# Kernel optimization log

Hardware: AMD Instinct MI355X
Metric: run time of the kernel (lower is better)

The kernel has to match this reference:

```python
import jax, jax.numpy as jnp
import numpy as np

B, S, D, H, OUT = 64, 2048, 1024, 300, 2
DROPOUT = 0.2


def setup_inputs() -> dict:
    key = jax.random.key(0)
    k_in, k_ids, k_pos, k_mask, k_w1, k_w2 = jax.random.split(key, 6)
    inputs = jax.random.normal(k_in, (B, S, D), dtype=jnp.float32)
    # token ids in [2, 32000); then plant a single '1' (EOS/pad marker) per row
    input_ids = jax.random.randint(k_ids, (B, S), 2, 32000, dtype=jnp.int64)
    eos_pos = jax.random.randint(k_pos, (B,), S // 2, S)
    input_ids = input_ids.at[jnp.arange(B), eos_pos].set(1)
    # realized Bernoulli(1 - dropout) token-keep mask, [B, S, 1]
    drop_mask = (jax.random.uniform(k_mask, (B, S, 1)) < (1.0 - DROPOUT)).astype(jnp.float32)
    W1 = jax.random.normal(k_w1, (H, D), dtype=jnp.float32) * 0.02
    b1 = jnp.zeros((H,), dtype=jnp.float32)
    W2 = jax.random.normal(k_w2, (OUT, H), dtype=jnp.float32) * 0.02
    b2 = jnp.zeros((OUT,), dtype=jnp.float32)
    return {"inputs": inputs, "input_ids": input_ids, "drop_mask": drop_mask,
            "W1": W1, "b1": b1, "W2": W2, "b2": b2}


def reference(inputs, input_ids, drop_mask, W1, b1, W2, b2):
    # end_ind[i] = first position where input_ids[i] == 1; fallback matches
    # the original's `except: end_ind = input_ids.shape[0]` (== batch size)
    is_end = input_ids == 1                              # [B, S]
    has_end = jnp.any(is_end, axis=1)                    # [B]
    first_end = jnp.argmax(is_end, axis=1)               # [B]
    end_ind = jnp.where(has_end, first_end, input_ids.shape[0])

    # masked, dropped segment-average over the first end_ind tokens
    valid = (jnp.arange(inputs.shape[1])[None, :] < end_ind[:, None])  # [B, S]
    weighted = inputs * drop_mask * valid[:, :, None].astype(inputs.dtype)
    euph = weighted.sum(axis=1) / end_ind[:, None].astype(inputs.dtype)  # [B, D]

    # 2-layer MLP with tanh
    hidden = jnp.tanh(euph @ W1.T + b1)
    out = hidden @ W2.T + b2                             # [B, 2]
    return out
```

## Files before the change

kernel.cpp:

```cpp
#include <hip/hip_runtime.h>
#include <math.h>

#define B 64
#define S 2048
#define D 1024
#define H 300
#define NOUT 2
#define NCHUNK 32
#define CHUNK_S (S / NCHUNK)

typedef float fx4 __attribute__((ext_vector_type(4)));

static __device__ __forceinline__ int imin(int a, int b) { return a < b ? a : b; }

__global__ __launch_bounds__(256) void end_kernel(const int* __restrict__ ids,
                                                  int* __restrict__ end_ind) {
    int b = blockIdx.x;
    int t = threadIdx.x;
    const int* row = ids + (size_t)b * S;
    int m = S;
    for (int s = t; s < S; s += 256) {
        if (row[s] == 1 && s < m) m = s;
    }
    __shared__ int red[256];
    red[t] = m;
    __syncthreads();
    for (int st = 128; st > 0; st >>= 1) {
        if (t < st) red[t] = imin(red[t], red[t + st]);
        __syncthreads();
    }
    if (t == 0) end_ind[b] = (red[0] < S) ? red[0] : B;
}

__global__ __launch_bounds__(256) void sum_partial_kernel(
        const float* __restrict__ inputs,
        const float* __restrict__ drop,
        const int* __restrict__ end_ind,
        float* __restrict__ partial ) {
    int chunk = blockIdx.x;
    int b = blockIdx.y;
    int t = threadIdx.x;

    __shared__ int   rows_l[CHUNK_S];
    __shared__ float w_l[CHUNK_S];
    __shared__ int   cnt_l;

    int e = end_ind[b];
    int s0 = chunk * CHUNK_S;
    int n = imin(s0 + CHUNK_S, e) - s0;

    if (t < 64) {
        float w = 0.f;
        if (t < n) w = drop[(size_t)b * S + s0 + t];
        unsigned long long mask = __ballot(w != 0.f);
        int pos = __popcll(mask & ((1ull << t) - 1ull));
        if (w != 0.f) { rows_l[pos] = t; w_l[pos] = w; }
        if (t == 0) cnt_l = __popcll(mask);
    }
    __syncthreads();

    int m = cnt_l;
    fx4 a0 = (fx4)(0.f);
    fx4 a1 = a0, a2 = a0, a3 = a0, a4 = a0, a5 = a0, a6 = a0, a7 = a0;

    const char* base = (const char*)inputs + (((size_t)b * S + s0) * D + 4 * (size_t)t) * sizeof(float);

    int i = 0;
    for (; i + 8 <= m; i += 8) {
        fx4 v0 = *(const fx4*)(base + ((size_t)rows_l[i + 0] << 12));
        fx4 v1 = *(const fx4*)(base + ((size_t)rows_l[i + 1] << 12));
        fx4 v2 = *(const fx4*)(base + ((size_t)rows_l[i + 2] << 12));
        fx4 v3 = *(const fx4*)(base + ((size_t)rows_l[i + 3] << 12));
        fx4 v4 = *(const fx4*)(base + ((size_t)rows_l[i + 4] << 12));
        fx4 v5 = *(const fx4*)(base + ((size_t)rows_l[i + 5] << 12));
        fx4 v6 = *(const fx4*)(base + ((size_t)rows_l[i + 6] << 12));
        fx4 v7 = *(const fx4*)(base + ((size_t)rows_l[i + 7] << 12));
        a0 += v0 * w_l[i + 0];
        a1 += v1 * w_l[i + 1];
        a2 += v2 * w_l[i + 2];
        a3 += v3 * w_l[i + 3];
        a4 += v4 * w_l[i + 4];
        a5 += v5 * w_l[i + 5];
        a6 += v6 * w_l[i + 6];
        a7 += v7 * w_l[i + 7];
    }
    for (; i < m; ++i) {
        fx4 v = *(const fx4*)(base + ((size_t)rows_l[i] << 12));
        a0 += v * w_l[i];
    }
    a0 = ((a0 + a1) + (a2 + a3)) + ((a4 + a5) + (a6 + a7));

    fx4* op = (fx4*)(partial + ((size_t)b * NCHUNK + chunk) * D) + t;
    *op = a0;
}

__global__ __launch_bounds__(256) void mlp_kernel(
        const float* __restrict__ partial,
        const int* __restrict__ end_ind,
        const float* __restrict__ W1, const float* __restrict__ b1,
        const float* __restrict__ W2, const float* __restrict__ b2,
        float* __restrict__ out) {
    int b = blockIdx.x;
    int t = threadIdx.x;
    int wave = t >> 6;
    int lane = t & 63;

    __shared__ fx4 x4[D / 4];
    __shared__ float hidden[H];
    __shared__ float red[256];

    float inv_e = 1.0f / (float)end_ind[b];
    {
        fx4 a = (fx4)(0.f);
        const fx4* p = (const fx4*)(partial + (size_t)b * NCHUNK * D) + t;
        for (int c = 0; c < NCHUNK; ++c, p += D / 4) {
            a += p[0];
        }
        x4[t] = a * inv_e;
    }
    __syncthreads();

    fx4 xr0 = x4[lane];
    fx4 xr1 = x4[lane + 64];
    fx4 xr2 = x4[lane + 128];
    fx4 xr3 = x4[lane + 192];

    for (int h = wave; h < H; h += 4) {
        const fx4* w = (const fx4*)(W1 + (size_t)h * D);
        fx4 acc = xr0 * w[lane]
                + xr1 * w[lane + 64]
                + xr2 * w[lane + 128]
                + xr3 * w[lane + 192];
        float d = acc.x + acc.y + acc.z + acc.w;
        #pragma unroll
        for (int mm = 32; mm > 0; mm >>= 1) d += __shfl_xor(d, mm, 64);
        if (lane == 0) hidden[h] = tanhf(d + b1[h]);
    }
    __syncthreads();

    for (int o = 0; o < NOUT; ++o) {
        float p = 0.f;
        for (int h = t; h < H; h += 256) p += hidden[h] * W2[(size_t)o * H + h];
        red[t] = p;
        __syncthreads();
        for (int st = 128; st > 0; st >>= 1) {
            if (t < st) red[t] += red[t + st];
            __syncthreads();
        }
        if (t == 0) out[b * NOUT + o] = red[0] + b2[o];
        __syncthreads();
    }
}

extern "C" void kernel_launch(void* const* d_in, const int* in_sizes, int n_in,
                              void* d_out, int out_size, void* d_ws, size_t ws_size,
                              hipStream_t stream) {
    const float* inputs = (const float*)d_in[0];
    const int*   ids    = (const int*)d_in[1];
    const float* drop   = (const float*)d_in[2];
    const float* W1     = (const float*)d_in[3];
    const float* b1v    = (const float*)d_in[4];
    const float* W2     = (const float*)d_in[5];
    const float* b2v    = (const float*)d_in[6];
    float* out = (float*)d_out;

    int*   end_ind = (int*)d_ws;
    float* partial = (float*)((char*)d_ws + 256);

    end_kernel<<<B, 256, 0, stream>>>(ids, end_ind);
    sum_partial_kernel<<<dim3(NCHUNK, B), 256, 0, stream>>>(inputs, drop, end_ind, partial);
    mlp_kernel<<<B, 256, 0, stream>>>(partial, end_ind, W1, b1v, W2, b2v, out);
}
```

Baseline: 733.2 us.

## Fuse end-index search into the sum kernel, halve chunk count, use nontemporal loads

Drops the separate end_kernel launch: every sum_partial block now scans the ids row itself, reduces the minimum with wave shuffles, and chunk 0 writes end_ind for the MLP kernel. Chunks grow from 64 to 128 rows, so row compaction is now built across two waves with a prefix offset. Input loads become nontemporal, and the MLP kernel runs with 512 threads so more W1 rows are handled in parallel. The cost is redundant id scans in every block and fewer, longer blocks, which may lower parallelism in the bandwidth-bound sum.

```diff
diff --git a/kernel.cpp b/kernel.cpp
--- a/kernel.cpp
+++ b/kernel.cpp
@@ -6,75 +6,79 @@
 #define D 1024
 #define H 300
 #define NOUT 2
-#define NCHUNK 32
+#define NCHUNK 16
 #define CHUNK_S (S / NCHUNK)
 
 typedef float fx4 __attribute__((ext_vector_type(4)));
 
 static __device__ __forceinline__ int imin(int a, int b) { return a < b ? a : b; }
 
-__global__ __launch_bounds__(256) void end_kernel(const int* __restrict__ ids,
-                                                  int* __restrict__ end_ind) {
-    int b = blockIdx.x;
-    int t = threadIdx.x;
-    const int* row = ids + (size_t)b * S;
-    int m = S;
-    for (int s = t; s < S; s += 256) {
-        if (row[s] == 1 && s < m) m = s;
-    }
-    __shared__ int red[256];
-    red[t] = m;
-    __syncthreads();
-    for (int st = 128; st > 0; st >>= 1) {
-        if (t < st) red[t] = imin(red[t], red[t + st]);
-        __syncthreads();
-    }
-    if (t == 0) end_ind[b] = (red[0] < S) ? red[0] : B;
-}
-
 __global__ __launch_bounds__(256) void sum_partial_kernel(
         const float* __restrict__ inputs,
+        const int* __restrict__ ids,
         const float* __restrict__ drop,
-        const int* __restrict__ end_ind,
+        int* __restrict__ end_ind,
         float* __restrict__ partial ) {
     int chunk = blockIdx.x;
     int b = blockIdx.y;
     int t = threadIdx.x;
+    int lane = t & 63;
+    int widx = t >> 6;
+
+    const int* idrow = ids + (size_t)b * S;
+    int m = S;
+    for (int s = t; s < S; s += 256) {
+        if (idrow[s] == 1 && s < m) m = s;
+    }
+    #pragma unroll
+    for (int off = 32; off > 0; off >>= 1) m = imin(m, __shfl_xor(m, off, 64));
+    __shared__ int wmin[4];
+    if (lane == 0) wmin[widx] = m;
+    __syncthreads();
+    int e_full = imin(imin(wmin[0], wmin[1]), imin(wmin[2], wmin[3]));
+    int e = (e_full < S) ? e_full : B;
+    if (t == 0 && chunk == 0) end_ind[b] = e;
+
+    int s0 = chunk * CHUNK_S;
+    int n = imin(s0 + CHUNK_S, e) - s0;
 
     __shared__ int   rows_l[CHUNK_S];
     __shared__ float w_l[CHUNK_S];
-    __shared__ int   cnt_l;
+    __shared__ int   wcnt[2];
 
-    int e = end_ind[b];
-    int s0 = chunk * CHUNK_S;
-    int n = imin(s0 + CHUNK_S, e) - s0;
-
-    if (t < 64) {
-        float w = 0.f;
-        if (t < n) w = drop[(size_t)b * S + s0 + t];
+    float w = 0.f;
+    int pos = 0;
+    if (t < CHUNK_S) {
+        w = (t < n) ? drop[(size_t)b * S + s0 + t] : 0.f;
         unsigned long long mask = __ballot(w != 0.f);
-        int pos = __popcll(mask & ((1ull << t) - 1ull));
-        if (w != 0.f) { rows_l[pos] = t; w_l[pos] = w; }
-        if (t == 0) cnt_l = __popcll(mask);
+        pos = __popcll(mask & ((1ull << lane) - 1ull));
+        if (lane == 0) wcnt[widx] = __popcll(mask);
     }
     __syncthreads();
+    int base0 = (widx == 1) ? wcnt[0] : 0;
+    if (t < CHUNK_S && w != 0.f) {
+        rows_l[base0 + pos] = t;
+        w_l[base0 + pos] = w;
+    }
+    int mtot = wcnt[0] + wcnt[1];
+    __syncthreads();
 
-    int m = cnt_l;
     fx4 a0 = (fx4)(0.f);
     fx4 a1 = a0, a2 = a0, a3 = a0, a4 = a0, a5 = a0, a6 = a0, a7 = a0;
 
-    const char* base = (const char*)inputs + (((size_t)b * S + s0) * D + 4 * (size_t)t) * sizeof(float);
+    const char* base = (const char*)inputs
+                     + (((size_t)b * S + s0) * D + 4 * (size_t)t) * sizeof(float);
 
     int i = 0;
-    for (; i + 8 <= m; i += 8) {
-        fx4 v0 = *(const fx4*)(base + ((size_t)rows_l[i + 0] << 12));
-        fx4 v1 = *(const fx4*)(base + ((size_t)rows_l[i + 1] << 12));
-        fx4 v2 = *(const fx4*)(base + ((size_t)rows_l[i + 2] << 12));
-        fx4 v3 = *(const fx4*)(base + ((size_t)rows_l[i + 3] << 12));
-        fx4 v4 = *(const fx4*)(base + ((size_t)rows_l[i + 4] << 12));
-        fx4 v5 = *(const fx4*)(base + ((size_t)rows_l[i + 5] << 12));
-        fx4 v6 = *(const fx4*)(base + ((size_t)rows_l[i + 6] << 12));
-        fx4 v7 = *(const fx4*)(base + ((size_t)rows_l[i + 7] << 12));
+    for (; i + 8 <= mtot; i += 8) {
+        fx4 v0 = __builtin_nontemporal_load((const fx4*)(base + ((size_t)rows_l[i + 0] << 12)));
+        fx4 v1 = __builtin_nontemporal_load((const fx4*)(base + ((size_t)rows_l[i + 1] << 12)));
+        fx4 v2 = __builtin_nontemporal_load((const fx4*)(base + ((size_t)rows_l[i + 2] << 12)));
+        fx4 v3 = __builtin_nontemporal_load((const fx4*)(base + ((size_t)rows_l[i + 3] << 12)));
+        fx4 v4 = __builtin_nontemporal_load((const fx4*)(base + ((size_t)rows_l[i + 4] << 12)));
+        fx4 v5 = __builtin_nontemporal_load((const fx4*)(base + ((size_t)rows_l[i + 5] << 12)));
+        fx4 v6 = __builtin_nontemporal_load((const fx4*)(base + ((size_t)rows_l[i + 6] << 12)));
+        fx4 v7 = __builtin_nontemporal_load((const fx4*)(base + ((size_t)rows_l[i + 7] << 12)));
         a0 += v0 * w_l[i + 0];
         a1 += v1 * w_l[i + 1];
         a2 += v2 * w_l[i + 2];
@@ -84,8 +88,8 @@
         a6 += v6 * w_l[i + 6];
         a7 += v7 * w_l[i + 7];
     }
-    for (; i < m; ++i) {
-        fx4 v = *(const fx4*)(base + ((size_t)rows_l[i] << 12));
+    for (; i < mtot; ++i) {
+        fx4 v = __builtin_nontemporal_load((const fx4*)(base + ((size_t)rows_l[i] << 12)));
         a0 += v * w_l[i];
     }
     a0 = ((a0 + a1) + (a2 + a3)) + ((a4 + a5) + (a6 + a7));
@@ -94,7 +98,7 @@
     *op = a0;
 }
 
-__global__ __launch_bounds__(256) void mlp_kernel(
+__global__ __launch_bounds__(512) void mlp_kernel(
         const float* __restrict__ partial,
         const int* __restrict__ end_ind,
         const float* __restrict__ W1, const float* __restrict__ b1,
@@ -107,10 +111,10 @@
 
     __shared__ fx4 x4[D / 4];
     __shared__ float hidden[H];
-    __shared__ float red[256];
+    __shared__ float red[512];
 
     float inv_e = 1.0f / (float)end_ind[b];
-    {
+    if (t < D / 4) {
         fx4 a = (fx4)(0.f);
         const fx4* p = (const fx4*)(partial + (size_t)b * NCHUNK * D) + t;
         for (int c = 0; c < NCHUNK; ++c, p += D / 4) {
@@ -125,7 +129,7 @@
     fx4 xr2 = x4[lane + 128];
     fx4 xr3 = x4[lane + 192];
 
-    for (int h = wave; h < H; h += 4) {
+    for (int h = wave; h < H; h += 8) {
         const fx4* w = (const fx4*)(W1 + (size_t)h * D);
         fx4 acc = xr0 * w[lane]
                 + xr1 * w[lane + 64]
@@ -140,10 +144,10 @@
 
     for (int o = 0; o < NOUT; ++o) {
         float p = 0.f;
-        for (int h = t; h < H; h += 256) p += hidden[h] * W2[(size_t)o * H + h];
+        for (int h = t; h < H; h += 512) p += hidden[h] * W2[(size_t)o * H + h];
         red[t] = p;
         __syncthreads();
-        for (int st = 128; st > 0; st >>= 1) {
+        for (int st = 256; st > 0; st >>= 1) {
             if (t < st) red[t] += red[t + st];
             __syncthreads();
         }
@@ -167,7 +171,6 @@
     int*   end_ind = (int*)d_ws;
     float* partial = (float*)((char*)d_ws + 256);
 
-    end_kernel<<<B, 256, 0, stream>>>(ids, end_ind);
-    sum_partial_kernel<<<dim3(NCHUNK, B), 256, 0, stream>>>(inputs, drop, end_ind, partial);
-    mlp_kernel<<<B, 256, 0, stream>>>(partial, end_ind, W1, b1v, W2, b2v, out);
+    sum_partial_kernel<<<dim3(NCHUNK, B), 256, 0, stream>>>(inputs, ids, drop, end_ind, partial);
+    mlp_kernel<<<B, 512, 0, stream>>>(partial, end_ind, W1, b1v, W2, b2v, out);
 }
```

Result: faster. 667.6 us (-9.0%).
